# Performance work log

Hardware: AMD Instinct MI355X
Metric: run time of the kernel (lower is better)

Reference implementation:

```python
import jax, jax.numpy as jnp
import numpy as np

BIT = 64
NUM_TRAIN = 100000
N_CLASS = 100
BATCH = 128
MU = 1.0
NU = 0.1
ETA = 55.0
DCC_ITER = 10


def setup_inputs() -> dict:
    key = jax.random.key(0)
    k1, k2, k3, k4, k5 = jax.random.split(key, 5)
    u = jax.random.normal(k1, (BATCH, BIT), dtype=jnp.float32)
    y = (jax.random.uniform(k2, (BATCH, N_CLASS)) < 0.1).astype(jnp.float32)
    ind = jnp.arange(BATCH, dtype=jnp.int32)  # unique column indices into num_train
    U = jax.random.normal(k3, (BIT, NUM_TRAIN), dtype=jnp.float32)
    B = jnp.sign(jax.random.normal(k4, (BIT, NUM_TRAIN), dtype=jnp.float32))  # +-1 codes
    Ybuf = (jax.random.uniform(k5, (N_CLASS, NUM_TRAIN)) < 0.1).astype(jnp.float32)
    return {"u": u, "y": y, "ind": ind, "U": U, "B": B, "Ybuf": Ybuf}


def _update_b_and_w(B, U, Ybuf):
    # Faithful DCC: dcc_iter outer iterations; within each, W from a ridge
    # solve, then sequential sign coordinate-descent over the `bit` rows of B.
    lam_eye = (NU / MU) * jnp.eye(BIT, dtype=B.dtype)
    W = None
    for _ in range(DCC_ITER):
        # W = inv(B B^T + (nu/mu) I) @ B @ Y^T  -> (bit, n_class)
        W = jnp.linalg.solve(B @ B.T + lam_eye, B @ Ybuf.T)
        P = W @ Ybuf + (ETA / MU) * U  # (bit, num_train); constant within inner loop

        def body(Bc, i):
            w = W[i]                         # (n_class,)
            Ww = W @ w                       # (bit,)
            # B_prime.T @ W_prime @ w == B.T @ (W @ w) - B[i] * (w . w)
            row = jnp.sign(P[i] - (Ww @ Bc - Bc[i] * (w @ w)))
            return Bc.at[i].set(row), None

        B, _ = jax.lax.scan(body, B, jnp.arange(BIT))
    return B, W


def reference(u, y, ind, U, B, Ybuf):
    # buffer updates: U gets detached u (torch uses u.t().data), Y gets y
    U = U.at[:, ind].set(jax.lax.stop_gradient(u).T)
    Ybuf = Ybuf.at[:, ind].set(y.T)
    B, W = _update_b_and_w(B, U, Ybuf)

    inner_product = (u @ U) * 0.5                       # (batch, num_train)
    s = (y @ Ybuf > 0).astype(u.dtype)                  # (batch, num_train)
    likelihood = jnp.log1p(jnp.exp(-jnp.abs(inner_product))) \
        + jnp.maximum(inner_product, 0.0) - s * inner_product
    likelihood_loss = jnp.mean(likelihood)
    cl_loss = jnp.mean((y.T - W.T @ B[:, ind]) ** 2)    # (n_class, batch)
    reg_loss = jnp.mean(W ** 2)
    return likelihood_loss + MU * cl_loss + NU * reg_loss
```

## Files before the change

kernel.cpp:

```cpp
#include <hip/hip_runtime.h>
#include <cstdint>
#include <cstddef>


#define NT 100000
#define WPR 1568
#define NWREAL 1563
#define NGRPP 1568
#define NJB 1563
#define ETA_MU 55.0f
#define LAM 0.1f

typedef unsigned long long u64;
typedef _Float16 half8 __attribute__((ext_vector_type(8)));
typedef _Float16 half4 __attribute__((ext_vector_type(4)));
typedef _Float16 half2v __attribute__((ext_vector_type(2)));
typedef float float4v __attribute__((ext_vector_type(4)));

__device__ inline float hsum8(half8 a) {
  half4 lo = __builtin_shufflevector(a, a, 0, 1, 2, 3);
  half4 hi = __builtin_shufflevector(a, a, 4, 5, 6, 7);
  half4 s4 = lo + hi;
  half2v l2 = __builtin_shufflevector(s4, s4, 0, 1);
  half2v h2 = __builtin_shufflevector(s4, s4, 2, 3);
  half2v s2 = l2 + h2;
  return (float)s2[0] + (float)s2[1];
}

__device__ inline u64 transpose64(u64 x, int lane) {
  const u64 ms[6] = {0x5555555555555555ull,0x3333333333333333ull,0x0F0F0F0F0F0F0F0Full,
                     0x00FF00FF00FF00FFull,0x0000FFFF0000FFFFull,0x00000000FFFFFFFFull};
#pragma unroll
  for (int si = 0; si < 6; ++si) {
    int s = 1 << si;
    u64 m = ms[si];
    u64 y = __shfl_xor(x, s, 64);
    if ((lane & s) == 0) x = (x & m) | ((y & m) << s);
    else                 x = (x & ~m) | ((y & ~m) >> s);
  }
  return x;
}

__device__ inline int wave_reduce_i32(int v) {
#pragma unroll
  for (int off = 32; off > 0; off >>= 1) v += __shfl_down(v, off, 64);
  return v;
}
__device__ inline double wave_reduce_f64(double v) {
#pragma unroll
  for (int off = 32; off > 0; off >>= 1) v += __shfl_down(v, off, 64);
  return v;
}

__global__ __launch_bounds__(256) void build_colmasks(
    const float* __restrict__ B, const float* __restrict__ Ybuf,
    u64* __restrict__ Bmask, u64* __restrict__ Ymask,
    signed char* __restrict__ owner, int* __restrict__ cflags) {
  if (blockIdx.x == 0 && threadIdx.x < 16) cflags[threadIdx.x] = 0;
  int j = blockIdx.x * 256 + threadIdx.x;
  if (j >= NT) return;
  owner[j] = (signed char)-1;
  u64 bm = 0;
#pragma unroll
  for (int i = 0; i < 64; ++i)
    bm |= ((u64)(B[(size_t)i * NT + j] > 0.0f)) << i;
  u64 m0 = 0, m1 = 0;
#pragma unroll
  for (int c = 0; c < 64; ++c)
    m0 |= ((u64)(Ybuf[(size_t)c * NT + j] > 0.5f)) << c;
#pragma unroll
  for (int c = 64; c < 100; ++c)
    m1 |= ((u64)(Ybuf[(size_t)c * NT + j] > 0.5f)) << (c - 64);
  Bmask[j] = bm;
  Ymask[2 * j] = m0;
  Ymask[2 * j + 1] = m1;
}

__global__ void scatter_y(const float* __restrict__ y, const int* __restrict__ ind,
                          u64* __restrict__ Ymask, u64* __restrict__ ybatch,
                          signed char* __restrict__ owner, int* __restrict__ popcY) {
  int b = threadIdx.x;
  if (b >= 128) return;
  if (b < 100) popcY[b] = 0;
  u64 m0 = 0, m1 = 0;
  for (int c = 0; c < 100; ++c) {
    bool v = y[b * 100 + c] > 0.5f;
    if (c < 64) m0 |= ((u64)v) << c;
    else        m1 |= ((u64)v) << (c - 64);
  }
  ybatch[2 * b] = m0;
  ybatch[2 * b + 1] = m1;
  int col = ind[b];
  Ymask[2 * col] = m0;
  Ymask[2 * col + 1] = m1;
  owner[col] = (signed char)b;
}

__global__ __launch_bounds__(256) void build_rows(
    const u64* __restrict__ Bmask, const u64* __restrict__ Ymask,
    u64* __restrict__ Brow, u64* __restrict__ Yrow, int* __restrict__ popcY) {
  int g = blockIdx.x * 4 + (threadIdx.x >> 6);
  int lane = threadIdx.x & 63;
  if (g >= NGRPP) return;
  int j = g * 64 + lane;
  bool act = j < NT;
  u64 bm = act ? Bmask[j] : 0ull;
  u64 y0 = act ? Ymask[2 * j] : 0ull;
  u64 y1 = act ? Ymask[2 * j + 1] : 0ull;
  u64 tb = transpose64(bm, lane);
  Brow[(size_t)lane * WPR + g] = tb;
  u64 t0 = transpose64(y0, lane);
  Yrow[(size_t)lane * WPR + g] = t0;
  atomicAdd(&popcY[lane], (int)__popcll(t0));
  u64 t1 = transpose64(y1, lane);
  if (lane < 36) {
    Yrow[(size_t)(64 + lane) * WPR + g] = t1;
    atomicAdd(&popcY[64 + lane], (int)__popcll(t1));
  }
}

__global__ __launch_bounds__(256, 4) void k1_sr(
    const u64* __restrict__ Brow, const u64* __restrict__ Yrow,
    int* __restrict__ S_part, int* __restrict__ R_part,
    int it, const int* __restrict__ cflags) {
  if (it > 0 && cflags[it - 1] == 0) return;
  int k = blockIdx.x;
  int q = blockIdx.y;
  int w0 = q * 196;
  int wv = threadIdx.x >> 6, lane = threadIdx.x & 63;
  u64 tmask = (lane < 4) ? ~0ull : 0ull;
  const u64* bk = Brow + (size_t)k * WPR + w0;
  u64 b0 = bk[lane], b1 = bk[lane + 64], b2 = bk[lane + 128];
  u64 b3 = bk[192 + (lane & 3)] & tmask;
  int sS[16];
#pragma unroll
  for (int m = 0; m < 16; ++m) {
    const u64* br = Brow + (size_t)(4 * m + wv) * WPR + w0;
    u64 x0 = br[lane], x1 = br[lane + 64], x2 = br[lane + 128];
    u64 x3 = br[192 + (lane & 3)] & tmask;
    sS[m] = __popcll(x0 ^ b0) + __popcll(x1 ^ b1) +
            __popcll(x2 ^ b2) + __popcll(x3 ^ b3);
  }
  int sR[25];
#pragma unroll
  for (int m = 0; m < 25; ++m) {
    const u64* yr = Yrow + (size_t)(4 * m + wv) * WPR + w0;
    u64 x0 = yr[lane], x1 = yr[lane + 64], x2 = yr[lane + 128];
    u64 x3 = yr[192 + (lane & 3)] & tmask;
    sR[m] = __popcll(x0 & b0) + __popcll(x1 & b1) +
            __popcll(x2 & b2) + __popcll(x3 & b3);
  }
#pragma unroll
  for (int off = 32; off > 0; off >>= 1) {
#pragma unroll
    for (int m = 0; m < 16; ++m) sS[m] += __shfl_down(sS[m], off, 64);
#pragma unroll
    for (int m = 0; m < 25; ++m) sR[m] += __shfl_down(sR[m], off, 64);
  }
  if (lane == 0) {
#pragma unroll
    for (int m = 0; m < 16; ++m)
      S_part[q * 4096 + k * 64 + 4 * m + wv] = sS[m];
#pragma unroll
    for (int m = 0; m < 25; ++m)
      R_part[q * 6400 + k * 100 + 4 * m + wv] = sR[m];
  }
}

__global__ __launch_bounds__(256, 1) void k2a_solve(
    const int* __restrict__ S_part, const int* __restrict__ R_part,
    const int* __restrict__ popcY, float* __restrict__ Wr,
    float* __restrict__ Wc, int it, const int* __restrict__ cflags) {
  if (it > 0 && cflags[it - 1] == 0) return;
  __shared__ short sEi[4096];
  __shared__ _Float16 sXa[64 * 32];
  __shared__ _Float16 sXb[64 * 32];
  int tid = threadIdx.x;
  int wv = tid >> 6, k = tid & 63;
  int b = blockIdx.x;
  const int qbase_t[4] = {0, 7, 14, 20};
  const int qcnt_t[4]  = {7, 7, 6, 6};
  int qbase = qbase_t[b], Q = qcnt_t[b];
  const int off7[4] = {0, 2, 4, 6}, cnt7[4] = {2, 2, 2, 1};
  const int off6[4] = {0, 2, 4, 5}, cnt6[4] = {2, 2, 1, 1};
  int woff = (Q == 7) ? off7[wv] : off6[wv];
  int wcnt = (Q == 7) ? cnt7[wv] : cnt6[wv];
  const float alpha = 1.0f / (100000.0f + LAM);
  for (int e = tid; e < 4096; e += 256) {
    int kk = e >> 6, ll = e & 63;
    int mm = 0;
#pragma unroll
    for (int qq = 0; qq < 8; ++qq) mm += S_part[qq * 4096 + e];
    int v = (kk == ll) ? 0 : (NT - 2 * mm);
    v = v > 32767 ? 32767 : (v < -32767 ? -32767 : v);
    sEi[kk * 64 + (ll ^ (kk & 31))] = (short)v;
  }
  float4 rr4[2], xf[2];
#pragma unroll
  for (int q = 0; q < 2; ++q) {
    if (q < wcnt) {
      float tmp[4];
#pragma unroll
      for (int e4 = 0; e4 < 4; ++e4) {
        int cg = 4 * (qbase + woff + q) + e4;
        float rv = 0.0f;
        if (cg < 100) {
          int rr = 0;
#pragma unroll
          for (int qq = 0; qq < 8; ++qq) rr += R_part[qq * 6400 + k * 100 + cg];
          rv = (float)(2 * rr - popcY[cg]);
        }
        tmp[e4] = rv;
      }
      rr4[q] = make_float4(tmp[0], tmp[1], tmp[2], tmp[3]);
      xf[q] = make_float4(alpha * tmp[0], alpha * tmp[1],
                          alpha * tmp[2], alpha * tmp[3]);
    }
  }
  if (wcnt == 2) {
    half8 h;
    h[0] = (_Float16)xf[0].x; h[1] = (_Float16)xf[0].y;
    h[2] = (_Float16)xf[0].z; h[3] = (_Float16)xf[0].w;
    h[4] = (_Float16)xf[1].x; h[5] = (_Float16)xf[1].y;
    h[6] = (_Float16)xf[1].z; h[7] = (_Float16)xf[1].w;
    *(half8*)&sXa[k * 32 + 4 * woff] = h;
  } else {
    half4 h;
    h[0] = (_Float16)xf[0].x; h[1] = (_Float16)xf[0].y;
    h[2] = (_Float16)xf[0].z; h[3] = (_Float16)xf[0].w;
    *(half4*)&sXa[k * 32 + 4 * woff] = h;
  }
  __syncthreads();
  _Float16* Xs = sXa;
  _Float16* Xd = sXb;
  for (int it2 = 0; it2 < 4; ++it2) {
    float4 a4[2];
#pragma unroll
    for (int q = 0; q < 2; ++q)
      if (q < wcnt) a4[q] = rr4[q];
    if (wcnt == 2) {
      for (int l = 0; l < 64; ++l) {
        float ev = (float)sEi[k * 64 + (l ^ (k & 31))];
        half8 x8 = *(const half8*)&Xs[l * 32 + 4 * woff];
        a4[0].x -= ev * (float)x8[0]; a4[0].y -= ev * (float)x8[1];
        a4[0].z -= ev * (float)x8[2]; a4[0].w -= ev * (float)x8[3];
        a4[1].x -= ev * (float)x8[4]; a4[1].y -= ev * (float)x8[5];
        a4[1].z -= ev * (float)x8[6]; a4[1].w -= ev * (float)x8[7];
      }
    } else {
      for (int l = 0; l < 64; ++l) {
        float ev = (float)sEi[k * 64 + (l ^ (k & 31))];
        half4 x4 = *(const half4*)&Xs[l * 32 + 4 * woff];
        a4[0].x -= ev * (float)x4[0]; a4[0].y -= ev * (float)x4[1];
        a4[0].z -= ev * (float)x4[2]; a4[0].w -= ev * (float)x4[3];
      }
    }
#pragma unroll
    for (int q = 0; q < 2; ++q) {
      if (q < wcnt) {
        xf[q] = make_float4(alpha * a4[q].x, alpha * a4[q].y,
                            alpha * a4[q].z, alpha * a4[q].w);
      }
    }
    if (it2 < 3) {
      if (wcnt == 2) {
        half8 h;
        h[0] = (_Float16)xf[0].x; h[1] = (_Float16)xf[0].y;
        h[2] = (_Float16)xf[0].z; h[3] = (_Float16)xf[0].w;
        h[4] = (_Float16)xf[1].x; h[5] = (_Float16)xf[1].y;
        h[6] = (_Float16)xf[1].z; h[7] = (_Float16)xf[1].w;
        *(half8*)&Xd[k * 32 + 4 * woff] = h;
      } else {
        half4 h;
        h[0] = (_Float16)xf[0].x; h[1] = (_Float16)xf[0].y;
        h[2] = (_Float16)xf[0].z; h[3] = (_Float16)xf[0].w;
        *(half4*)&Xd[k * 32 + 4 * woff] = h;
      }
      __syncthreads();
      _Float16* t = Xs; Xs = Xd; Xd = t;
    }
  }
#pragma unroll
  for (int q = 0; q < 2; ++q) {
    if (q < wcnt) {
      float v4[4] = {xf[q].x, xf[q].y, xf[q].z, xf[q].w};
#pragma unroll
      for (int e4 = 0; e4 < 4; ++e4) {
        int cg = 4 * (qbase + woff + q) + e4;
        if (cg < 100) {
          Wr[k * 100 + cg] = v4[e4];
          Wc[cg * 64 + k] = v4[e4];
        }
      }
    }
  }
}

__global__ __launch_bounds__(256, 1) void k2b_gram(
    const float* __restrict__ Wr, float* __restrict__ G,
    int it, const int* __restrict__ cflags) {
  if (it > 0 && cflags[it - 1] == 0) return;
  __shared__ float sX[6400];
  int tid = threadIdx.x, wv = tid >> 6, k = tid & 63;
  for (int t = tid; t < 6400; t += 256) sX[t] = Wr[t];
  __syncthreads();
  float4 xl[25];
#pragma unroll
  for (int q = 0; q < 25; ++q) xl[q] = *(const float4*)&sX[k * 100 + 4 * q];
#pragma unroll
  for (int ii = 0; ii < 4; ++ii) {
    int i = blockIdx.x * 16 + wv * 4 + ii;
    const float4* xi = (const float4*)&sX[i * 100];
    float d0 = 0.f, d1 = 0.f, d2 = 0.f, d3 = 0.f;
#pragma unroll
    for (int q = 0; q < 25; ++q) {
      float4 a = xi[q];
      d0 += xl[q].x * a.x; d1 += xl[q].y * a.y;
      d2 += xl[q].z * a.z; d3 += xl[q].w * a.w;
    }
    G[i * 64 + k] = (d0 + d1) + (d2 + d3);
  }
}

__global__ __launch_bounds__(256, 2) void k3_gs(
    const float* __restrict__ U, const float* __restrict__ u,
    const signed char* __restrict__ owner, const float* __restrict__ Wc,
    const float* __restrict__ Gm, u64* __restrict__ Bmask,
    u64* __restrict__ Brow, const u64* __restrict__ Ymask,
    int it, int* __restrict__ cflags) {
  if (it > 0 && cflags[it - 1] == 0) return;
  __shared__ _Float16 sWh[100 * 72];
  __shared__ _Float16 sGh[64 * 64];
  __shared__ float sGd[64];
  for (int t = threadIdx.x; t < 6400; t += 256) {
    int c = t >> 6, i = t & 63;
    sWh[c * 72 + i] = (_Float16)Wc[t];
  }
  for (int t = threadIdx.x; t < 4096; t += 256) sGh[t] = (_Float16)Gm[t];
  if (threadIdx.x < 64) sGd[threadIdx.x] = Gm[threadIdx.x * 65];
  __syncthreads();
  int g = blockIdx.x * 4 + (threadIdx.x >> 6);
  int lane = threadIdx.x & 63;
  int j = g * 64 + lane;
  bool act = j < NT;
  int jc = act ? j : NT - 1;
  int ow = owner[jc];
  float p[64];
  if (ow >= 0) {
#pragma unroll
    for (int i = 0; i < 64; ++i) p[i] = ETA_MU * u[ow * 64 + i];
  } else {
#pragma unroll
    for (int i = 0; i < 64; ++i) p[i] = ETA_MU * U[(size_t)i * NT + jc];
  }
  u64 y0 = Ymask[2 * jc], y1 = Ymask[2 * jc + 1];
  half8 pw[8];
#pragma unroll
  for (int t = 0; t < 8; ++t) pw[t] = (half8)(_Float16)0.0f;
  u64 mm = y0;
  while (mm) {
    int c = __builtin_ctzll(mm); mm &= mm - 1;
    const half8* wr = (const half8*)&sWh[c * 72];
#pragma unroll
    for (int t = 0; t < 8; ++t) pw[t] += wr[t];
  }
  mm = y1;
  while (mm) {
    int c = 64 + __builtin_ctzll(mm); mm &= mm - 1;
    const half8* wr = (const half8*)&sWh[c * 72];
#pragma unroll
    for (int t = 0; t < 8; ++t) pw[t] += wr[t];
  }
#pragma unroll
  for (int t = 0; t < 8; ++t)
#pragma unroll
    for (int e = 0; e < 8; ++e)
      p[8 * t + e] += (float)pw[t][e];
  u64 bm = Bmask[jc];
  half8 bfh[8];
#pragma unroll
  for (int t = 0; t < 8; ++t)
#pragma unroll
    for (int e = 0; e < 8; ++e)
      bfh[t][e] = ((bm >> (8 * t + e)) & 1ull) ? (_Float16)1.0f : (_Float16)-1.0f;
  half8 qv[8];
#pragma unroll
  for (int t = 0; t < 8; ++t) qv[t] = (half8)(_Float16)0.0f;
#pragma unroll
  for (int i = 0; i < 64; ++i) {
    const half8* gr = (const half8*)&sGh[i * 64];
    _Float16 bi = bfh[i >> 3][i & 7];
#pragma unroll
    for (int t = 0; t < 8; ++t) qv[t] += gr[t] * bi;
  }
#pragma unroll
  for (int i = 0; i < 64; ++i) {
    _Float16 ob = bfh[i >> 3][i & 7];
    float val = p[i] - (float)qv[i >> 3][i & 7] + sGd[i] * (float)ob;
    _Float16 nb = (val > 0.0f) ? (_Float16)1.0f : (_Float16)-1.0f;
    bool ch = (nb != ob);
    if (__any(ch)) {
      _Float16 dl = ch ? (_Float16)(nb + nb) : (_Float16)0.0f;
      const half8* gr = (const half8*)&sGh[i * 64];
#pragma unroll
      for (int t = 0; t < 8; ++t) qv[t] += gr[t] * dl;
      bfh[i >> 3][i & 7] = nb;
    }
  }
  u64 nm = 0;
#pragma unroll
  for (int t = 0; t < 8; ++t)
#pragma unroll
    for (int e = 0; e < 8; ++e)
      if (bfh[t][e] > (_Float16)0.0f) nm |= 1ull << (8 * t + e);
  if (!act) nm = 0;
  bool ch = act && (nm != bm);
  if (__any(ch) && lane == 0) cflags[it] = 1;
  if (act) Bmask[j] = nm;
  u64 tb = transpose64(nm, lane);
  Brow[(size_t)lane * WPR + g] = tb;
}

__global__ __launch_bounds__(256, 4) void l1_like(
    const float* __restrict__ U, const float* __restrict__ u,
    const signed char* __restrict__ owner, const u64* __restrict__ Ymask,
    const u64* __restrict__ ybatch, double* __restrict__ partial) {
  __shared__ _Float16 shu[8192];
  __shared__ u64 sy[256];
  __shared__ double wred[4];
  int tid = threadIdx.x;
  for (int e = tid; e < 1024; e += 256) {
    int b = e >> 3, k8 = e & 7;
    const float4* src = (const float4*)&u[b * 64 + k8 * 8];
    float4 f0 = src[0], f1 = src[1];
    half8 h;
    h[0] = (_Float16)f0.x; h[1] = (_Float16)f0.y;
    h[2] = (_Float16)f0.z; h[3] = (_Float16)f0.w;
    h[4] = (_Float16)f1.x; h[5] = (_Float16)f1.y;
    h[6] = (_Float16)f1.z; h[7] = (_Float16)f1.w;
    *(half8*)&shu[b * 64 + ((k8 ^ (b & 7)) * 8)] = h;
  }
  if (tid < 256) sy[tid] = ybatch[tid];
  __syncthreads();
  int wv = tid >> 6, lane = tid & 63;
  int n = lane & 15, q = lane >> 4;
  int j = blockIdx.x * 64 + wv * 16 + n;
  bool actj = j < NT;
  int jc = actj ? j : NT - 1;
  int ow = owner[jc];
  half8 bf0, bf1;
#pragma unroll
  for (int t = 0; t < 8; ++t) {
    int k = q * 8 + t;
    bf0[t] = (_Float16)U[(size_t)k * NT + jc];
    bf1[t] = (_Float16)U[(size_t)(k + 32) * NT + jc];
  }
  if (ow >= 0) {
#pragma unroll
    for (int t = 0; t < 8; ++t) {
      bf0[t] = (_Float16)u[ow * 64 + q * 8 + t];
      bf1[t] = (_Float16)u[ow * 64 + 32 + q * 8 + t];
    }
  }
  u64 ym0 = Ymask[2 * jc], ym1 = Ymask[2 * jc + 1];
  float lsum = 0.0f;
#pragma unroll
  for (int t8 = 0; t8 < 8; ++t8) {
    int brow = t8 * 16 + n;
    half8 a0 = *(const half8*)&shu[brow * 64 + ((q ^ (brow & 7)) * 8)];
    half8 a1 = *(const half8*)&shu[brow * 64 + (((q + 4) ^ (brow & 7)) * 8)];
    float4v c = {0.f, 0.f, 0.f, 0.f};
    c = __builtin_amdgcn_mfma_f32_16x16x32_f16(a0, bf0, c, 0, 0, 0);
    c = __builtin_amdgcn_mfma_f32_16x16x32_f16(a1, bf1, c, 0, 0, 0);
#pragma unroll
    for (int r = 0; r < 4; ++r) {
      int b = t8 * 16 + q * 4 + r;
      float ip = 0.5f * c[r];
      u64 yb0 = sy[2 * b], yb1 = sy[2 * b + 1];
      bool s = ((yb0 & ym0) | (yb1 & ym1)) != 0ull;
      float a = fabsf(ip);
      lsum += __logf(1.0f + __expf(-a)) + fmaxf(ip, 0.0f) - (s ? ip : 0.0f);
    }
  }
  if (!actj) lsum = 0.0f;
  double lsd = wave_reduce_f64((double)lsum);
  if (lane == 0) wred[wv] = lsd;
  __syncthreads();
  if (tid == 0)
    partial[blockIdx.x] = wred[0] + wred[1] + wred[2] + wred[3];
}

__global__ __launch_bounds__(256) void l2_fin(
    const float* __restrict__ Wr, const float* __restrict__ y,
    const int* __restrict__ ind, const u64* __restrict__ Bmask,
    const double* __restrict__ partial, float* __restrict__ out) {
  __shared__ float sw[6400];
  __shared__ u64 sbm[128];
  __shared__ double dred[12];
  int tid = threadIdx.x;
  for (int t = tid; t < 6400; t += 256) sw[t] = Wr[t];
  if (tid < 128) sbm[tid] = Bmask[ind[tid]];
  __syncthreads();
  double cls = 0.0, regs = 0.0, l1s = 0.0;
  for (int e = tid; e < 12800; e += 256) {
    int c = e >> 7, b = e & 127;
    u64 bm = sbm[b];
    float s = 0.0f;
#pragma unroll
    for (int i = 0; i < 64; ++i) {
      float w = sw[i * 100 + c];
      s += ((bm >> i) & 1ull) ? w : -w;
    }
    float d = y[b * 100 + c] - s;
    cls += (double)(d * d);
  }
  for (int e = tid; e < 6400; e += 256) {
    float w = sw[e];
    regs += (double)(w * w);
  }
  for (int t = tid; t < NJB; t += 256) l1s += partial[t];
  cls = wave_reduce_f64(cls);
  regs = wave_reduce_f64(regs);
  l1s = wave_reduce_f64(l1s);
  int wv = tid >> 6;
  if ((tid & 63) == 0) { dred[wv] = cls; dred[4 + wv] = regs; dred[8 + wv] = l1s; }
  __syncthreads();
  if (tid == 0) {
    double c = dred[0] + dred[1] + dred[2] + dred[3];
    double r = dred[4] + dred[5] + dred[6] + dred[7];
    double l = dred[8] + dred[9] + dred[10] + dred[11];
    out[0] = (float)(l * (1.0 / 12800000.0) + c * (1.0 / 12800.0) +
                     r * (0.1 / 6400.0));
  }
}

extern "C" void kernel_launch(void* const* d_in, const int* in_sizes, int n_in,
                              void* d_out, int out_size, void* d_ws, size_t ws_size,
                              hipStream_t stream) {
  const float* u    = (const float*)d_in[0];
  const float* y    = (const float*)d_in[1];
  const int*   ind  = (const int*)d_in[2];
  const float* U    = (const float*)d_in[3];
  const float* B    = (const float*)d_in[4];
  const float* Ybuf = (const float*)d_in[5];
  char* ws = (char*)d_ws;
  int* cflags        = (int*)ws;
  u64* Bmask         = (u64*)(ws + 256);
  u64* Ymask         = (u64*)(ws + 800256);
  u64* Brow          = (u64*)(ws + 2400256);
  u64* Yrow          = (u64*)(ws + 3203072);
  u64* ybatch        = (u64*)(ws + 4457472);
  int* popcY         = (int*)(ws + 4459520);
  int* S_part        = (int*)(ws + 4460032);
  int* R_part        = (int*)(ws + 4591104);
  float* Wr          = (float*)(ws + 4795904);
  float* Wc          = (float*)(ws + 4821504);
  float* G           = (float*)(ws + 4847104);
  signed char* owner = (signed char*)(ws + 4863488);
  double* partial    = (double*)(ws + 4963520);

  build_colmasks<<<391, 256, 0, stream>>>(B, Ybuf, Bmask, Ymask, owner, cflags);
  scatter_y<<<1, 128, 0, stream>>>(y, ind, Ymask, ybatch, owner, popcY);
  build_rows<<<392, 256, 0, stream>>>(Bmask, Ymask, Brow, Yrow, popcY);
  for (int it = 0; it < 10; ++it) {
    k1_sr<<<dim3(64, 8), 256, 0, stream>>>(Brow, Yrow, S_part, R_part, it, cflags);
    k2a_solve<<<4, 256, 0, stream>>>(S_part, R_part, popcY, Wr, Wc, it, cflags);
    k2b_gram<<<4, 256, 0, stream>>>(Wr, G, it, cflags);
    k3_gs<<<392, 256, 0, stream>>>(U, u, owner, Wc, G, Bmask, Brow, Ymask, it, cflags);
  }
  l1_like<<<NJB, 256, 0, stream>>>(U, u, owner, Ymask, ybatch, partial);
  l2_fin<<<1, 256, 0, stream>>>(Wr, y, ind, Bmask, partial, (float*)d_out);
}
```

Measured before the change: 588.5 us.

## Compute W·y and G·b per column with MFMA in the Gauss-Seidel kernel

The sign coordinate-descent kernel used to build the W·Y projection with a per-lane loop over set label bits and the initial G·b product with scalar half-vector FMAs. Both are now computed as 16x16x32 fp16 MFMA tiles per wave, with W transposed and G padded in shared memory. Results are staged through a per-wave shared buffer and added into an fp32 residual vector. The sequential update now keeps that residual in fp32 and subtracts G rows on each flip, in place of a half-precision q vector. This adds shared memory and a block barrier, and rounds the MFMA outputs to fp16, which may change which signs flip.

```diff
diff --git a/kernel.cpp b/kernel.cpp
--- a/kernel.cpp
+++ b/kernel.cpp
@@ -16,16 +16,6 @@
 typedef _Float16 half4 __attribute__((ext_vector_type(4)));
 typedef _Float16 half2v __attribute__((ext_vector_type(2)));
 typedef float float4v __attribute__((ext_vector_type(4)));
-
-__device__ inline float hsum8(half8 a) {
-  half4 lo = __builtin_shufflevector(a, a, 0, 1, 2, 3);
-  half4 hi = __builtin_shufflevector(a, a, 4, 5, 6, 7);
-  half4 s4 = lo + hi;
-  half2v l2 = __builtin_shufflevector(s4, s4, 0, 1);
-  half2v h2 = __builtin_shufflevector(s4, s4, 2, 3);
-  half2v s2 = l2 + h2;
-  return (float)s2[0] + (float)s2[1];
-}
 
 __device__ inline u64 transpose64(u64 x, int lane) {
   const u64 ms[6] = {0x5555555555555555ull,0x3333333333333333ull,0x0F0F0F0F0F0F0F0Full,
@@ -329,93 +319,126 @@
     u64* __restrict__ Brow, const u64* __restrict__ Ymask,
     int it, int* __restrict__ cflags) {
   if (it > 0 && cflags[it - 1] == 0) return;
-  __shared__ _Float16 sWh[100 * 72];
-  __shared__ _Float16 sGh[64 * 64];
+  __shared__ _Float16 sWt[64 * 136];
+  __shared__ _Float16 sGr[64 * 72];
   __shared__ float sGd[64];
-  for (int t = threadIdx.x; t < 6400; t += 256) {
-    int c = t >> 6, i = t & 63;
-    sWh[c * 72 + i] = (_Float16)Wc[t];
-  }
-  for (int t = threadIdx.x; t < 4096; t += 256) sGh[t] = (_Float16)Gm[t];
-  if (threadIdx.x < 64) sGd[threadIdx.x] = Gm[threadIdx.x * 65];
-  __syncthreads();
-  int g = blockIdx.x * 4 + (threadIdx.x >> 6);
-  int lane = threadIdx.x & 63;
+  __shared__ _Float16 sQx[4 * 64 * 68];
+  int tid = threadIdx.x;
+  for (int t = tid; t < 8192; t += 256) {
+    int i = t & 63, c = t >> 6;
+    sWt[i * 136 + c] = (c < 100) ? (_Float16)Wc[c * 64 + i] : (_Float16)0.0f;
+  }
+  for (int t = tid; t < 4096; t += 256) {
+    int i = t >> 6, k = t & 63;
+    sGr[i * 72 + k] = (_Float16)Gm[t];
+  }
+  if (tid < 64) sGd[tid] = Gm[tid * 65];
+  __syncthreads();
+  int wv = tid >> 6, lane = tid & 63;
+  int g = blockIdx.x * 4 + wv;
+  int n15 = lane & 15, quad = lane >> 4;
   int j = g * 64 + lane;
   bool act = j < NT;
   int jc = act ? j : NT - 1;
+  u64 bm = Bmask[jc];
+  u64 y0 = Ymask[2 * jc], y1 = Ymask[2 * jc + 1];
+  half8 aW[4][4], aG[4][2];
+#pragma unroll
+  for (int mt = 0; mt < 4; ++mt) {
+    int rb = mt * 16 + n15;
+#pragma unroll
+    for (int kt = 0; kt < 4; ++kt)
+      aW[mt][kt] = *(const half8*)&sWt[rb * 136 + kt * 32 + quad * 8];
+#pragma unroll
+    for (int kt = 0; kt < 2; ++kt)
+      aG[mt][kt] = *(const half8*)&sGr[rb * 72 + kt * 32 + quad * 8];
+  }
+  _Float16* xq = &sQx[wv * 64 * 68];
+  int c0q = quad * 8;
+#pragma unroll
+  for (int nt = 0; nt < 4; ++nt) {
+    int src = nt * 16 + n15;
+    u64 cy0 = __shfl(y0, src, 64);
+    u64 cy1 = __shfl(y1, src, 64);
+    u64 cbm = __shfl(bm, src, 64);
+    half8 yf[4], bf[2];
+#pragma unroll
+    for (int kt = 0; kt < 2; ++kt) {
+      int c0 = kt * 32 + c0q;
+      u64 w = cy0 >> c0;
+      w |= (c0 ? (cy1 << ((64 - c0) & 63)) : 0ull);
+#pragma unroll
+      for (int e = 0; e < 8; ++e)
+        yf[kt][e] = ((w >> e) & 1ull) ? (_Float16)1.0f : (_Float16)0.0f;
+    }
+#pragma unroll
+    for (int kt = 2; kt < 4; ++kt) {
+      int c0 = (kt - 2) * 32 + c0q;
+      u64 w = cy1 >> c0;
+#pragma unroll
+      for (int e = 0; e < 8; ++e)
+        yf[kt][e] = ((w >> e) & 1ull) ? (_Float16)1.0f : (_Float16)0.0f;
+    }
+#pragma unroll
+    for (int kt = 0; kt < 2; ++kt) {
+      int c0 = kt * 32 + c0q;
+      u64 w = cbm >> c0;
+#pragma unroll
+      for (int e = 0; e < 8; ++e)
+        bf[kt][e] = ((w >> e) & 1ull) ? (_Float16)-1.0f : (_Float16)1.0f;
+    }
+#pragma unroll
+    for (int mt = 0; mt < 4; ++mt) {
+      float4v c = {0.f, 0.f, 0.f, 0.f};
+#pragma unroll
+      for (int kt = 0; kt < 4; ++kt)
+        c = __builtin_amdgcn_mfma_f32_16x16x32_f16(aW[mt][kt], yf[kt], c, 0, 0, 0);
+#pragma unroll
+      for (int kt = 0; kt < 2; ++kt)
+        c = __builtin_amdgcn_mfma_f32_16x16x32_f16(aG[mt][kt], bf[kt], c, 0, 0, 0);
+      half4 hs;
+      hs[0] = (_Float16)c[0]; hs[1] = (_Float16)c[1];
+      hs[2] = (_Float16)c[2]; hs[3] = (_Float16)c[3];
+      *(half4*)&xq[(nt * 16 + n15) * 68 + mt * 16 + quad * 4] = hs;
+    }
+  }
+  __syncthreads();
   int ow = owner[jc];
-  float p[64];
+  float r[64];
   if (ow >= 0) {
 #pragma unroll
-    for (int i = 0; i < 64; ++i) p[i] = ETA_MU * u[ow * 64 + i];
+    for (int i = 0; i < 64; ++i) r[i] = ETA_MU * u[ow * 64 + i];
   } else {
 #pragma unroll
-    for (int i = 0; i < 64; ++i) p[i] = ETA_MU * U[(size_t)i * NT + jc];
-  }
-  u64 y0 = Ymask[2 * jc], y1 = Ymask[2 * jc + 1];
-  half8 pw[8];
-#pragma unroll
-  for (int t = 0; t < 8; ++t) pw[t] = (half8)(_Float16)0.0f;
-  u64 mm = y0;
-  while (mm) {
-    int c = __builtin_ctzll(mm); mm &= mm - 1;
-    const half8* wr = (const half8*)&sWh[c * 72];
-#pragma unroll
-    for (int t = 0; t < 8; ++t) pw[t] += wr[t];
-  }
-  mm = y1;
-  while (mm) {
-    int c = 64 + __builtin_ctzll(mm); mm &= mm - 1;
-    const half8* wr = (const half8*)&sWh[c * 72];
-#pragma unroll
-    for (int t = 0; t < 8; ++t) pw[t] += wr[t];
-  }
-#pragma unroll
-  for (int t = 0; t < 8; ++t)
-#pragma unroll
-    for (int e = 0; e < 8; ++e)
-      p[8 * t + e] += (float)pw[t][e];
-  u64 bm = Bmask[jc];
-  half8 bfh[8];
-#pragma unroll
-  for (int t = 0; t < 8; ++t)
-#pragma unroll
-    for (int e = 0; e < 8; ++e)
-      bfh[t][e] = ((bm >> (8 * t + e)) & 1ull) ? (_Float16)1.0f : (_Float16)-1.0f;
-  half8 qv[8];
-#pragma unroll
-  for (int t = 0; t < 8; ++t) qv[t] = (half8)(_Float16)0.0f;
+    for (int i = 0; i < 64; ++i) r[i] = ETA_MU * U[(size_t)i * NT + jc];
+  }
+#pragma unroll
+  for (int t = 0; t < 16; ++t) {
+    half4 hq = *(const half4*)&xq[lane * 68 + t * 4];
+#pragma unroll
+    for (int e = 0; e < 4; ++e) r[t * 4 + e] += (float)hq[e];
+  }
+  u64 cm = bm;
 #pragma unroll
   for (int i = 0; i < 64; ++i) {
-    const half8* gr = (const half8*)&sGh[i * 64];
-    _Float16 bi = bfh[i >> 3][i & 7];
-#pragma unroll
-    for (int t = 0; t < 8; ++t) qv[t] += gr[t] * bi;
-  }
-#pragma unroll
-  for (int i = 0; i < 64; ++i) {
-    _Float16 ob = bfh[i >> 3][i & 7];
-    float val = p[i] - (float)qv[i >> 3][i & 7] + sGd[i] * (float)ob;
-    _Float16 nb = (val > 0.0f) ? (_Float16)1.0f : (_Float16)-1.0f;
+    bool ob = (cm >> i) & 1ull;
+    float val = r[i] + (ob ? sGd[i] : -sGd[i]);
+    bool nb = val > 0.0f;
     bool ch = (nb != ob);
     if (__any(ch)) {
-      _Float16 dl = ch ? (_Float16)(nb + nb) : (_Float16)0.0f;
-      const half8* gr = (const half8*)&sGh[i * 64];
-#pragma unroll
-      for (int t = 0; t < 8; ++t) qv[t] += gr[t] * dl;
-      bfh[i >> 3][i & 7] = nb;
-    }
-  }
-  u64 nm = 0;
-#pragma unroll
-  for (int t = 0; t < 8; ++t)
-#pragma unroll
-    for (int e = 0; e < 8; ++e)
-      if (bfh[t][e] > (_Float16)0.0f) nm |= 1ull << (8 * t + e);
-  if (!act) nm = 0;
-  bool ch = act && (nm != bm);
-  if (__any(ch) && lane == 0) cflags[it] = 1;
+      float dl = ch ? (nb ? 2.0f : -2.0f) : 0.0f;
+#pragma unroll
+      for (int t = 0; t < 8; ++t) {
+        half8 gr = *(const half8*)&sGr[i * 72 + t * 8];
+#pragma unroll
+        for (int e = 0; e < 8; ++e) r[t * 8 + e] -= (float)gr[e] * dl;
+      }
+      if (ch) cm ^= (1ull << i);
+    }
+  }
+  u64 nm = act ? cm : 0ull;
+  bool chg = act && (nm != bm);
+  if (__any(chg) && lane == 0) cflags[it] = 1;
   if (act) Bmask[j] = nm;
   u64 tb = transpose64(nm, lane);
   Brow[(size_t)lane * WPR + g] = tb;
```

Measured after the change: 778.5 us. 32.3% more time.
